# Kernel optimization log

Hardware: AMD Instinct MI355X
Metric: run time of the kernel (lower is better)

## Reference

```python
import jax, jax.numpy as jnp
import numpy as np

B, L, D = 8, 1024, 512
NB = 4              # num_blocks
DIN = 2 * D         # mamba expand=2
N = 16              # d_state
DTR = 32            # dt_rank = ceil(D/16)
DCONV = 4           # mamba depthwise conv kernel
FF = 2 * D          # ffn_expand=2
EPS = 1e-5


def setup_inputs() -> dict:
    key = jax.random.key(0)
    ks = iter(jax.random.split(key, 64))

    def rnd(shape, s=0.02):
        return jax.random.normal(next(ks), shape, jnp.float32) * s

    p = {}
    p["x"] = jax.random.normal(next(ks), (B, L, D), jnp.float32)
    # TemporalConvBlock (Conv1d D->D, k=3, pad=1, groups=1) + LayerNorm
    p["tconv_w"] = rnd((D, D, 3), 0.05)
    p["tconv_b"] = jnp.zeros((D,), jnp.float32)
    p["tnorm_w"] = jnp.ones((D,), jnp.float32)
    p["tnorm_b"] = jnp.zeros((D,), jnp.float32)
    # per-block params, stacked on leading NB axis
    p["ln1_w"] = jnp.ones((NB, D), jnp.float32)
    p["ln1_b"] = jnp.zeros((NB, D), jnp.float32)
    p["in_proj_w"] = rnd((NB, 2 * DIN, D))          # no bias (mamba default)
    p["conv_w"] = rnd((NB, DIN, 1, DCONV), 0.1)     # depthwise causal conv
    p["conv_b"] = jnp.zeros((NB, DIN), jnp.float32)
    p["x_proj_w"] = rnd((NB, DTR + 2 * N, DIN))     # no bias
    p["dt_proj_w"] = rnd((NB, DIN, DTR), 0.1)
    p["dt_proj_b"] = jnp.log(jnp.expm1(jnp.full((NB, DIN), 0.01, jnp.float32)))
    p["A_log"] = jnp.tile(jnp.log(jnp.arange(1, N + 1, dtype=jnp.float32))[None, None, :], (NB, DIN, 1))
    p["D_param"] = jnp.ones((NB, DIN), jnp.float32)
    p["out_proj_w"] = rnd((NB, D, DIN))             # no bias
    p["ln2_w"] = jnp.ones((NB, D), jnp.float32)
    p["ln2_b"] = jnp.zeros((NB, D), jnp.float32)
    p["ffn_w1"] = rnd((NB, FF, D))
    p["ffn_b1"] = jnp.zeros((NB, FF), jnp.float32)
    p["ffn_w2"] = rnd((NB, D, FF))
    p["ffn_b2"] = jnp.zeros((NB, D), jnp.float32)
    return p


def _ln(x, w, b):
    mu = jnp.mean(x, -1, keepdims=True)
    v = jnp.mean(jnp.square(x - mu), -1, keepdims=True)
    return (x - mu) * jax.lax.rsqrt(v + EPS) * w + b


def _selective_scan(u, dt, A, Bm, C, Dp):
    # u, dt: (B,L,DIN); A: (DIN,N); Bm, C: (B,L,N); Dp: (DIN,)
    def step(h, inp):
        u_t, dt_t, B_t, C_t = inp                      # (B,DIN),(B,DIN),(B,N),(B,N)
        dA = jnp.exp(dt_t[..., None] * A)              # (B,DIN,N)
        dBu = dt_t[..., None] * B_t[:, None, :] * u_t[..., None]
        h = dA * h + dBu
        y = jnp.einsum('bdn,bn->bd', h, C_t)
        return h, y

    h0 = jnp.zeros((u.shape[0], A.shape[0], A.shape[1]), u.dtype)
    xs = (u.swapaxes(0, 1), dt.swapaxes(0, 1), Bm.swapaxes(0, 1), C.swapaxes(0, 1))
    _, ys = jax.lax.scan(step, h0, xs)                 # ys: (L,B,DIN)
    return ys.swapaxes(0, 1) + u * Dp


def _mamba(x, in_w, cw, cb, xpw, dtw, dtb, A_log, Dp, ow):
    xz = jnp.einsum('bld,ed->ble', x, in_w)            # (B,L,2*DIN)
    u, z = jnp.split(xz, 2, axis=-1)
    # causal depthwise conv over time
    uc = u.swapaxes(1, 2)                              # (B,DIN,L)
    uc = jax.lax.conv_general_dilated(
        uc, cw, (1,), [(DCONV - 1, 0)],
        feature_group_count=DIN, dimension_numbers=('NCH', 'OIH', 'NCH'))
    uc = uc + cb[None, :, None]
    u = jax.nn.silu(uc.swapaxes(1, 2))                 # (B,L,DIN)
    xdb = jnp.einsum('bld,ed->ble', u, xpw)            # (B,L,DTR+2N)
    dtr, Bm, C = jnp.split(xdb, [DTR, DTR + N], axis=-1)
    dt = jax.nn.softplus(jnp.einsum('blr,dr->bld', dtr, dtw) + dtb)
    A = -jnp.exp(A_log)
    y = _selective_scan(u, dt, A, Bm, C, Dp)
    y = y * jax.nn.silu(z)
    return jnp.einsum('bld,ed->ble', y, ow)


def reference(x, tconv_w, tconv_b, tnorm_w, tnorm_b, ln1_w, ln1_b, in_proj_w,
              conv_w, conv_b, x_proj_w, dt_proj_w, dt_proj_b, A_log, D_param,
              out_proj_w, ln2_w, ln2_b, ffn_w1, ffn_b1, ffn_w2, ffn_b2):
    # TemporalConvBlock (dropout = identity in eval)
    hc = jax.lax.conv_general_dilated(
        x.swapaxes(1, 2), tconv_w, (1,), [(1, 1)],
        dimension_numbers=('NCH', 'OIH', 'NCH'))
    hc = (hc + tconv_b[None, :, None]).swapaxes(1, 2)
    h = _ln(hc + x, tnorm_w, tnorm_b)
    # stacked MambaWithFFN blocks
    for i in range(NB):
        h = h + _mamba(_ln(h, ln1_w[i], ln1_b[i]), in_proj_w[i], conv_w[i],
                       conv_b[i], x_proj_w[i], dt_proj_w[i], dt_proj_b[i],
                       A_log[i], D_param[i], out_proj_w[i])
        hn = _ln(h, ln2_w[i], ln2_b[i])
        ff = jax.nn.gelu(jnp.einsum('bld,fd->blf', hn, ffn_w1[i]) + ffn_b1[i],
                         approximate=False)
        h = h + jnp.einsum('blf,df->bld', ff, ffn_w2[i]) + ffn_b2[i]
    return h
```

## Files before the change

kernel.cpp:

```cpp
#include <hip/hip_runtime.h>
#include <hip/hip_bf16.h>
#include <math.h>

#define B_ 8
#define L_ 1024
#define D_ 512
#define NB_ 4
#define DIN_ 1024
#define NST_ 16
#define DTR_ 32
#define FF_ 1024
#define EPS_LN 1e-5f
#define M_ (B_ * L_)

#define SC_G 16
#define SC_C 32
#define SC_LEN (L_ / SC_C)

typedef __attribute__((ext_vector_type(8))) short short8;
typedef __attribute__((ext_vector_type(4))) float f32x4;

static __device__ __forceinline__ ushort f2bf(float f) {
  union { float f; unsigned u; } v; v.f = f;
  unsigned r = v.u + 0x7FFFu + ((v.u >> 16) & 1u);
  return (ushort)(r >> 16);
}
static __device__ __forceinline__ float bf2f(ushort u) {
  union { unsigned u; float f; } v; v.u = ((unsigned)u) << 16;
  return v.f;
}

static __device__ __forceinline__ void gll16(const void* g, void* l) {
  __builtin_amdgcn_global_load_lds(
      (const __attribute__((address_space(1))) void*)g,
      (__attribute__((address_space(3))) void*)l, 16, 0, 0);
}

template <int BM, int EPI, int OUTB>
__global__ __launch_bounds__(256) void mgemm2_k(
    const ushort* __restrict__ A, const ushort* __restrict__ W,
    const float* __restrict__ bias, void* __restrict__ Cp,
    float* __restrict__ C2, int M, int N, int K, int lda, int ldc)
{
  constexpr int MI = BM / 32;
  __shared__ ushort As[BM * 64];
  __shared__ ushort Bs[128 * 64];
  const int tid = threadIdx.x;
  const int lane = tid & 63;
  const int wid = tid >> 6;
  const int wm = (wid >> 1) * (BM / 2);
  const int wn = (wid & 1) * 64;
  const int bm = blockIdx.y * BM;
  const int bn = blockIdx.x * 128;
  const int fr = lane & 15;
  const int kq = lane >> 4;

  f32x4 acc[MI][4];
#pragma unroll
  for (int i = 0; i < MI; ++i)
#pragma unroll
    for (int j = 0; j < 4; ++j) acc[i][j] = (f32x4)0.f;

  for (int k0 = 0; k0 < K; k0 += 64) {
#pragma unroll
    for (int it = 0; it < BM / 32; ++it) {
      const int sb = it * 4096 + wid * 1024 + lane * 16;
      const int row = sb >> 7;
      const int js = (sb >> 4) & 7;
      const int j2 = js ^ (row & 7);
      gll16(A + (size_t)(bm + row) * lda + k0 + j2 * 8,
            (char*)As + it * 4096 + wid * 1024);
    }
#pragma unroll
    for (int it = 0; it < 4; ++it) {
      const int sb = it * 4096 + wid * 1024 + lane * 16;
      const int row = sb >> 7;
      const int js = (sb >> 4) & 7;
      const int j2 = js ^ (row & 7);
      gll16(W + (size_t)(bn + row) * K + k0 + j2 * 8,
            (char*)Bs + it * 4096 + wid * 1024);
    }
    __syncthreads();
#pragma unroll
    for (int kk = 0; kk < 2; ++kk) {
      short8 af[MI], bf[4];
#pragma unroll
      for (int mi = 0; mi < MI; ++mi) {
        const int r = wm + mi * 16 + fr;
        af[mi] = *(const short8*)&As[r * 64 + ((((kk << 2) + kq) ^ (r & 7)) << 3)];
      }
#pragma unroll
      for (int ni = 0; ni < 4; ++ni) {
        const int r = wn + ni * 16 + fr;
        bf[ni] = *(const short8*)&Bs[r * 64 + ((((kk << 2) + kq) ^ (r & 7)) << 3)];
      }
#pragma unroll
      for (int mi = 0; mi < MI; ++mi)
#pragma unroll
        for (int ni = 0; ni < 4; ++ni)
          acc[mi][ni] = __builtin_amdgcn_mfma_f32_16x16x32_bf16(
              af[mi], bf[ni], acc[mi][ni], 0, 0, 0);
    }
    __syncthreads();
  }

#pragma unroll
  for (int mi = 0; mi < MI; ++mi) {
#pragma unroll
    for (int ni = 0; ni < 4; ++ni) {
#pragma unroll
      for (int r = 0; r < 4; ++r) {
        const int gm = bm + wm + mi * 16 + (lane >> 4) * 4 + r;
        const int gn = bn + wn + ni * 16 + fr;
        float v = acc[mi][ni][r];
        if (EPI == 6) {
          if (gn < DIN_) {
            v += bias[gn];
            v = (v > 20.f) ? v : __logf(1.f + __expf(v));
            ((float*)Cp)[(size_t)gm * DIN_ + gn] = v;
          } else if (gn < DIN_ + 2 * NST_) {
            C2[(size_t)gm * (2 * NST_) + (gn - DIN_)] = v;
          }
        } else {
          if (EPI == 2 || EPI == 5) v += bias[gn];
          if (EPI == 2) v = 0.5f * v * (1.f + erff(v * 0.70710678118654752f));
          if (OUTB) {
            ((ushort*)Cp)[(size_t)gm * ldc + gn] = f2bf(v);
          } else {
            float* pc = (float*)Cp + (size_t)gm * ldc + gn;
            if (EPI == 4 || EPI == 5) v += *pc;
            *pc = v;
          }
        }
      }
    }
  }
}

template <int MODE, int EPI, int BN, int OUTB>
__global__ __launch_bounds__(256) void mgemm_k(
    const float* __restrict__ Ap, const ushort* __restrict__ W,
    const float* __restrict__ bias, void* __restrict__ Cp,
    int M, int N, int K, int lda, int ldc)
{
  constexpr int FN = BN / 32;
  __shared__ ushort As[128 * 32];
  __shared__ ushort Bs[BN * 32];
  const int tid = threadIdx.x;
  const int lane = tid & 63;
  const int wid = tid >> 6;
  const int wm = (wid >> 1) * 64;
  const int wn = (wid & 1) * (BN / 2);
  const int bm = blockIdx.y * 128;
  const int bn = blockIdx.x * BN;
  const int fr = lane & 15;
  const int kq = lane >> 4;

  f32x4 acc[4][FN];
#pragma unroll
  for (int i = 0; i < 4; ++i)
#pragma unroll
    for (int j = 0; j < FN; ++j) acc[i][j] = (f32x4)0.f;

  for (int k0 = 0; k0 < K; k0 += 32) {
#pragma unroll
    for (int it = 0; it < 2; ++it) {
      const int idx = tid + it * 256;
      const int row = idx >> 2;
      const int j = idx & 3;
      short8 s;
      float4 v0, v1;
      if (MODE == 0) {
        const float* p = Ap + (size_t)(bm + row) * lda + k0 + j * 8;
        v0 = *(const float4*)p; v1 = *(const float4*)(p + 4);
      } else {
        const int kk = k0 + j * 8;
        const int tap = kk >> 9;
        const int dcol = kk & 511;
        const int m = bm + row;
        const int l = (m & (L_ - 1)) + tap - 1;
        if (l >= 0 && l < L_) {
          const float* p = Ap + (size_t)(m - (m & (L_ - 1)) + l) * D_ + dcol;
          v0 = *(const float4*)p; v1 = *(const float4*)(p + 4);
        } else {
          v0 = make_float4(0.f, 0.f, 0.f, 0.f); v1 = v0;
        }
      }
      s[0] = (short)f2bf(v0.x); s[1] = (short)f2bf(v0.y);
      s[2] = (short)f2bf(v0.z); s[3] = (short)f2bf(v0.w);
      s[4] = (short)f2bf(v1.x); s[5] = (short)f2bf(v1.y);
      s[6] = (short)f2bf(v1.z); s[7] = (short)f2bf(v1.w);
      *(short8*)&As[row * 32 + ((j ^ ((row >> 1) & 3)) << 3)] = s;
    }
#pragma unroll
    for (int it = 0; it < BN / 64; ++it) {
      const int idx = tid + it * 256;
      const int row = idx >> 2;
      const int j = idx & 3;
      short8 s = *(const short8*)(W + (size_t)(bn + row) * K + k0 + j * 8);
      *(short8*)&Bs[row * 32 + ((j ^ ((row >> 1) & 3)) << 3)] = s;
    }
    __syncthreads();
    short8 af[4], bfr[FN];
#pragma unroll
    for (int mi = 0; mi < 4; ++mi) {
      const int r = wm + mi * 16 + fr;
      af[mi] = *(const short8*)&As[r * 32 + ((kq ^ ((r >> 1) & 3)) << 3)];
    }
#pragma unroll
    for (int ni = 0; ni < FN; ++ni) {
      const int r = wn + ni * 16 + fr;
      bfr[ni] = *(const short8*)&Bs[r * 32 + ((kq ^ ((r >> 1) & 3)) << 3)];
    }
#pragma unroll
    for (int mi = 0; mi < 4; ++mi)
#pragma unroll
      for (int ni = 0; ni < FN; ++ni)
        acc[mi][ni] = __builtin_amdgcn_mfma_f32_16x16x32_bf16(
            af[mi], bfr[ni], acc[mi][ni], 0, 0, 0);
    __syncthreads();
  }

#pragma unroll
  for (int mi = 0; mi < 4; ++mi) {
#pragma unroll
    for (int ni = 0; ni < FN; ++ni) {
#pragma unroll
      for (int r = 0; r < 4; ++r) {
        const int gm = bm + wm + mi * 16 + (lane >> 4) * 4 + r;
        const int gn = bn + wn + ni * 16 + fr;
        float v = acc[mi][ni][r];
        if (EPI == 1) v += bias[gn];
        if (OUTB) ((ushort*)Cp)[(size_t)gm * ldc + gn] = f2bf(v);
        else ((float*)Cp)[(size_t)gm * ldc + gn] = v;
      }
    }
  }
}

template <int INB, int OUTB>
__global__ __launch_bounds__(256) void ln_k(
    const void* __restrict__ inp, const float* __restrict__ res,
    const float* __restrict__ w, const float* __restrict__ b,
    void* __restrict__ outp)
{
  const int row = blockIdx.x;
  const int t = threadIdx.x;
  float v0, v1;
  if (INB) {
    const ushort* p = (const ushort*)inp + (size_t)row * D_;
    v0 = bf2f(p[t]); v1 = bf2f(p[t + 256]);
  } else {
    const float* p = (const float*)inp + (size_t)row * D_;
    v0 = p[t]; v1 = p[t + 256];
  }
  if (res) {
    const float* r = res + (size_t)row * D_;
    v0 += r[t]; v1 += r[t + 256];
  }
  float s = v0 + v1;
  float sq = v0 * v0 + v1 * v1;
#pragma unroll
  for (int m = 1; m < 64; m <<= 1) {
    s += __shfl_xor(s, m, 64);
    sq += __shfl_xor(sq, m, 64);
  }
  __shared__ float ss[4], qq[4];
  const int wid = t >> 6;
  if ((t & 63) == 0) { ss[wid] = s; qq[wid] = sq; }
  __syncthreads();
  s = ss[0] + ss[1] + ss[2] + ss[3];
  sq = qq[0] + qq[1] + qq[2] + qq[3];
  const float mu = s * (1.f / (float)D_);
  const float var = sq * (1.f / (float)D_) - mu * mu;
  const float rs = rsqrtf(var + EPS_LN);
  const float o0 = (v0 - mu) * rs * w[t] + b[t];
  const float o1 = (v1 - mu) * rs * w[t + 256] + b[t + 256];
  if (OUTB) {
    ushort* o = (ushort*)outp + (size_t)row * D_;
    o[t] = f2bf(o0); o[t + 256] = f2bf(o1);
  } else {
    float* o = (float*)outp + (size_t)row * D_;
    o[t] = o0; o[t + 256] = o1;
  }
}

__global__ __launch_bounds__(256) void dwconv_k(
    const ushort* __restrict__ xz, const float* __restrict__ cw,
    const float* __restrict__ cb, ushort* __restrict__ u)
{
  const int idx = blockIdx.x * 256 + threadIdx.x;
  const int c8 = idx & (DIN_ / 8 - 1);
  const int bl = idx >> 7;
  const int l = bl & (L_ - 1);
  const int b0 = bl - l;
  const int c0 = c8 * 8;
  float s[8], w[8][4];
#pragma unroll
  for (int j = 0; j < 8; ++j) {
    s[j] = cb[c0 + j];
    const float4 wv = *(const float4*)(cw + (c0 + j) * 4);
    w[j][0] = wv.x; w[j][1] = wv.y; w[j][2] = wv.z; w[j][3] = wv.w;
  }
#pragma unroll
  for (int k = 0; k < 4; ++k) {
    const int ll = l + k - 3;
    if (ll >= 0) {
      const short8 v = *(const short8*)(xz + (size_t)(b0 + ll) * (2 * DIN_) + c0);
#pragma unroll
      for (int j = 0; j < 8; ++j)
        s[j] = fmaf(bf2f((ushort)v[j]), w[j][k], s[j]);
    }
  }
  short8 o;
#pragma unroll
  for (int j = 0; j < 8; ++j) {
    const float t = s[j] / (1.f + __expf(-s[j]));
    o[j] = (short)f2bf(t);
  }
  *(short8*)(u + (size_t)idx * 8) = o;
}

template <bool FAST>
static __device__ __forceinline__ void dAcalc(float dtv, float A0,
                                              const float* A, float* dA)
{
  if (FAST) {
    const float e = __expf(dtv * A0);
    dA[0] = e;
#pragma unroll
    for (int n = 1; n < 16; ++n) dA[n] = dA[n - 1] * e;
  } else {
#pragma unroll
    for (int n = 0; n < 16; ++n) dA[n] = __expf(dtv * A[n]);
  }
}

template <bool FAST>
static __device__ __forceinline__ void scan_run(
    const float* __restrict__ dt, ushort* __restrict__ u,
    const float* __restrict__ BC, const ushort* __restrict__ xz,
    const float* __restrict__ A_log,
    const float* A, const float A0, const float Dpd,
    float (*Hs)[SC_G][NST_ + 1], float (*Ss)[SC_G],
    const int tid, const int g, const int c, const int d0, const int d,
    const size_t base)
{
  const int l0 = c * SC_LEN;
  float h[16];
#pragma unroll
  for (int n = 0; n < 16; ++n) h[n] = 0.f;
  float S = 0.f;

  {
    size_t row = base + l0;
    float dtv = dt[row * DIN_ + d];
    float uv = bf2f(u[row * DIN_ + d]);
    float Bv[16];
    *(float4*)&Bv[0]  = *(const float4*)(BC + row * 32);
    *(float4*)&Bv[4]  = *(const float4*)(BC + row * 32 + 4);
    *(float4*)&Bv[8]  = *(const float4*)(BC + row * 32 + 8);
    *(float4*)&Bv[12] = *(const float4*)(BC + row * 32 + 12);
    for (int i = 0; i < SC_LEN; ++i) {
      float ndt = 0.f, nu = 0.f;
      float NBv[16];
      if (i + 1 < SC_LEN) {
        const size_t nrow = row + 1;
        ndt = dt[nrow * DIN_ + d];
        nu = bf2f(u[nrow * DIN_ + d]);
        *(float4*)&NBv[0]  = *(const float4*)(BC + nrow * 32);
        *(float4*)&NBv[4]  = *(const float4*)(BC + nrow * 32 + 4);
        *(float4*)&NBv[8]  = *(const float4*)(BC + nrow * 32 + 8);
        *(float4*)&NBv[12] = *(const float4*)(BC + nrow * 32 + 12);
      }
      S += dtv;
      const float du = dtv * uv;
      float dA[16];
      dAcalc<FAST>(dtv, A0, A, dA);
#pragma unroll
      for (int n = 0; n < 16; ++n)
        h[n] = fmaf(dA[n], h[n], du * Bv[n]);
      dtv = ndt; uv = nu;
#pragma unroll
      for (int n = 0; n < 16; ++n) Bv[n] = NBv[n];
      row += 1;
    }
  }
#pragma unroll
  for (int n = 0; n < 16; ++n) Hs[c][g][n] = h[n];
  Ss[c][g] = S;
  __syncthreads();

  if (tid < SC_G * NST_) {
    const int gg = tid >> 4;
    const int n2 = tid & 15;
    const float An = -expf(A_log[(d0 + gg) * NST_ + n2]);
    float hin = 0.f;
#pragma unroll
    for (int cc = 0; cc < SC_C; ++cc) {
      const float tmp = Hs[cc][gg][n2];
      const float P = __expf(An * Ss[cc][gg]);
      Hs[cc][gg][n2] = hin;
      hin = tmp + P * hin;
    }
  }
  __syncthreads();

#pragma unroll
  for (int n = 0; n < 16; ++n) h[n] = Hs[c][g][n];
  {
    size_t row = base + l0;
    float dtv = dt[row * DIN_ + d];
    float uv = bf2f(u[row * DIN_ + d]);
    float zv = bf2f(xz[row * (2 * DIN_) + DIN_ + d]);
    float Bv[16], Cv[16];
    *(float4*)&Bv[0]  = *(const float4*)(BC + row * 32);
    *(float4*)&Bv[4]  = *(const float4*)(BC + row * 32 + 4);
    *(float4*)&Bv[8]  = *(const float4*)(BC + row * 32 + 8);
    *(float4*)&Bv[12] = *(const float4*)(BC + row * 32 + 12);
    *(float4*)&Cv[0]  = *(const float4*)(BC + row * 32 + 16);
    *(float4*)&Cv[4]  = *(const float4*)(BC + row * 32 + 20);
    *(float4*)&Cv[8]  = *(const float4*)(BC + row * 32 + 24);
    *(float4*)&Cv[12] = *(const float4*)(BC + row * 32 + 28);
    for (int i = 0; i < SC_LEN; ++i) {
      float ndt = 0.f, nu = 0.f, nz = 0.f;
      float NBv[16], NCv[16];
      if (i + 1 < SC_LEN) {
        const size_t nrow = row + 1;
        ndt = dt[nrow * DIN_ + d];
        nu = bf2f(u[nrow * DIN_ + d]);
        nz = bf2f(xz[nrow * (2 * DIN_) + DIN_ + d]);
        *(float4*)&NBv[0]  = *(const float4*)(BC + nrow * 32);
        *(float4*)&NBv[4]  = *(const float4*)(BC + nrow * 32 + 4);
        *(float4*)&NBv[8]  = *(const float4*)(BC + nrow * 32 + 8);
        *(float4*)&NBv[12] = *(const float4*)(BC + nrow * 32 + 12);
        *(float4*)&NCv[0]  = *(const float4*)(BC + nrow * 32 + 16);
        *(float4*)&NCv[4]  = *(const float4*)(BC + nrow * 32 + 20);
        *(float4*)&NCv[8]  = *(const float4*)(BC + nrow * 32 + 24);
        *(float4*)&NCv[12] = *(const float4*)(BC + nrow * 32 + 28);
      }
      const float du = dtv * uv;
      float y = uv * Dpd;
      float dA[16];
      dAcalc<FAST>(dtv, A0, A, dA);
#pragma unroll
      for (int n = 0; n < 16; ++n) {
        h[n] = fmaf(dA[n], h[n], du * Bv[n]);
        y = fmaf(h[n], Cv[n], y);
      }
      y *= zv / (1.f + __expf(-zv));
      u[row * DIN_ + d] = f2bf(y);
      dtv = ndt; uv = nu; zv = nz;
#pragma unroll
      for (int n = 0; n < 16; ++n) { Bv[n] = NBv[n]; Cv[n] = NCv[n]; }
      row += 1;
    }
  }
}

__global__ __launch_bounds__(512) void scan5_k(
    const float* __restrict__ dt, ushort* u,
    const float* __restrict__ BC, const ushort* __restrict__ xz,
    const float* __restrict__ A_log, const float* __restrict__ Dp)
{
  const int tid = threadIdx.x;
  const int g = tid & (SC_G - 1);
  const int c = tid >> 4;
  const int b = blockIdx.x >> 6;
  const int d0 = (blockIdx.x & 63) * SC_G;
  const int d = d0 + g;

  __shared__ float Hs[SC_C][SC_G][NST_ + 1];
  __shared__ float Ss[SC_C][SC_G];
  __shared__ int slow;
  if (tid == 0) slow = 0;
  __syncthreads();

  float A[16];
#pragma unroll
  for (int n = 0; n < 16; ++n) A[n] = -expf(A_log[d * NST_ + n]);
  const float A0 = A[0];
  bool myfast = true;
#pragma unroll
  for (int n = 1; n < 16; ++n)
    myfast = myfast && (fabsf(A[n] - (float)(n + 1) * A0) <= 1e-3f * fabsf(A[n]));
  if (!myfast) slow = 1;
  __syncthreads();
  const float Dpd = Dp[d];
  const size_t base = (size_t)b * L_;

  if (slow == 0)
    scan_run<true>(dt, u, BC, xz, A_log, A, A0, Dpd, Hs, Ss, tid, g, c, d0, d, base);
  else
    scan_run<false>(dt, u, BC, xz, A_log, A, A0, Dpd, Hs, Ss, tid, g, c, d0, d, base);
}

__global__ __launch_bounds__(256) void cvt_k(const float* __restrict__ in,
                                             ushort* __restrict__ out, int n8)
{
  const int i = blockIdx.x * 256 + threadIdx.x;
  if (i >= n8) return;
  const float4 a = *(const float4*)(in + (size_t)i * 8);
  const float4 b = *(const float4*)(in + (size_t)i * 8 + 4);
  short8 s;
  s[0] = (short)f2bf(a.x); s[1] = (short)f2bf(a.y);
  s[2] = (short)f2bf(a.z); s[3] = (short)f2bf(a.w);
  s[4] = (short)f2bf(b.x); s[5] = (short)f2bf(b.y);
  s[6] = (short)f2bf(b.z); s[7] = (short)f2bf(b.w);
  *(short8*)(out + (size_t)i * 8) = s;
}

__global__ __launch_bounds__(256) void twt_k(const float* __restrict__ in,
                                             ushort* __restrict__ out)
{
  const int i = blockIdx.x * 256 + threadIdx.x;
  if (i >= D_ * D_ * 3) return;
  const int o = i / (D_ * 3);
  const int rem = i - o * (D_ * 3);
  const int d = rem / 3;
  const int tap = rem - d * 3;
  out[(size_t)o * (D_ * 3) + tap * D_ + d] = f2bf(in[i]);
}

__global__ __launch_bounds__(256) void xpT_k(const float* __restrict__ xpw,
                                             ushort* __restrict__ out)
{
  const int i = blockIdx.x * 256 + threadIdx.x;
  if (i >= DIN_ * DTR_) return;
  const int k = i >> 5;
  const int r = i & 31;
  out[i] = f2bf(xpw[(size_t)r * DIN_ + k]);
}

__global__ __launch_bounds__(256) void pack_k(const float* __restrict__ wc,
                                              const float* __restrict__ xpw,
                                              ushort* __restrict__ wbig)
{
  const int i = blockIdx.x * 256 + threadIdx.x;
  if (i >= 1152 * 1024) return;
  const int r = i >> 10;
  const int k = i & 1023;
  float v;
  if (r < 1024) v = wc[i];
  else if (r < 1056) v = xpw[(size_t)(DTR_ + r - 1024) * DIN_ + k];
  else v = 0.f;
  wbig[i] = f2bf(v);
}

extern "C" void kernel_launch(void* const* d_in, const int* in_sizes, int n_in,
                              void* d_out, int out_size, void* d_ws, size_t ws_size,
                              hipStream_t stream)
{
  const float* x         = (const float*)d_in[0];
  const float* tconv_w   = (const float*)d_in[1];
  const float* tconv_b   = (const float*)d_in[2];
  const float* tnorm_w   = (const float*)d_in[3];
  const float* tnorm_b   = (const float*)d_in[4];
  const float* ln1_w     = (const float*)d_in[5];
  const float* ln1_b     = (const float*)d_in[6];
  const float* in_proj_w = (const float*)d_in[7];
  const float* conv_w    = (const float*)d_in[8];
  const float* conv_b    = (const float*)d_in[9];
  const float* x_proj_w  = (const float*)d_in[10];
  const float* dt_proj_w = (const float*)d_in[11];
  const float* dt_proj_b = (const float*)d_in[12];
  const float* A_log     = (const float*)d_in[13];
  const float* D_param   = (const float*)d_in[14];
  const float* out_proj_w= (const float*)d_in[15];
  const float* ln2_w     = (const float*)d_in[16];
  const float* ln2_b     = (const float*)d_in[17];
  const float* ffn_w1    = (const float*)d_in[18];
  const float* ffn_b1    = (const float*)d_in[19];
  const float* ffn_w2    = (const float*)d_in[20];
  const float* ffn_b2    = (const float*)d_in[21];

  float* h = (float*)d_out;

  char* p = (char*)d_ws;
  ushort* wTT  = (ushort*)p; p += (size_t)512 * 1536 * 2;
  ushort* wIP  = (ushort*)p; p += (size_t)4 * 2048 * 512 * 2;
  ushort* wOP  = (ushort*)p; p += (size_t)4 * 512 * 1024 * 2;
  ushort* wF1  = (ushort*)p; p += (size_t)4 * 1024 * 512 * 2;
  ushort* wF2  = (ushort*)p; p += (size_t)4 * 512 * 1024 * 2;
  ushort* xpwT = (ushort*)p; p += (size_t)4 * 1024 * 32 * 2;
  ushort* wBig = (ushort*)p; p += (size_t)4 * 1152 * 1024 * 2;
  float*  wcT  = (float*)p;  p += (size_t)1024 * 1024 * 4;
  ushort* xin  = (ushort*)p; p += (size_t)M_ * 512 * 2;
  ushort* xzb  = (ushort*)p; p += (size_t)M_ * 2048 * 2;
  ushort* ubuf = (ushort*)p; p += (size_t)M_ * 1024 * 2;
  float*  bc   = (float*)p;  p += (size_t)M_ * 32 * 4;
  float*  dtb  = (float*)p;  p += (size_t)M_ * 1024 * 4;
  ushort* ff   = (ushort*)p; p += (size_t)M_ * 1024 * 2;

  const dim3 blk(256);

  cvt_k<<<dim3(4 * 2048 * 512 / 8 / 256), blk, 0, stream>>>(in_proj_w, wIP, 4 * 2048 * 512 / 8);
  cvt_k<<<dim3(4 * 512 * 1024 / 8 / 256), blk, 0, stream>>>(out_proj_w, wOP, 4 * 512 * 1024 / 8);
  cvt_k<<<dim3(4 * 1024 * 512 / 8 / 256), blk, 0, stream>>>(ffn_w1, wF1, 4 * 1024 * 512 / 8);
  cvt_k<<<dim3(4 * 512 * 1024 / 8 / 256), blk, 0, stream>>>(ffn_w2, wF2, 4 * 512 * 1024 / 8);
  twt_k<<<dim3((D_ * D_ * 3 + 255) / 256), blk, 0, stream>>>(tconv_w, wTT);
  for (int i = 0; i < NB_; ++i)
    xpT_k<<<dim3(DIN_ * DTR_ / 256), blk, 0, stream>>>(
        x_proj_w + (size_t)i * 64 * DIN_, xpwT + (size_t)i * DIN_ * DTR_);
  for (int i = 0; i < NB_; ++i) {
    mgemm_k<0, 0, 128, 0><<<dim3(8, 8), blk, 0, stream>>>(
        dt_proj_w + (size_t)i * DIN_ * DTR_, xpwT + (size_t)i * DIN_ * DTR_,
        nullptr, wcT, 1024, 1024, 32, 32, 1024);
    pack_k<<<dim3(1152 * 1024 / 256), blk, 0, stream>>>(
        wcT, x_proj_w + (size_t)i * 64 * DIN_, wBig + (size_t)i * 1152 * 1024);
  }

  mgemm_k<1, 1, 64, 1><<<dim3(8, 64), blk, 0, stream>>>(
      x, wTT, tconv_b, xin, M_, 512, 1536, 0, 512);
  ln_k<1, 0><<<dim3(M_), blk, 0, stream>>>(xin, x, tnorm_w, tnorm_b, h);

  for (int i = 0; i < NB_; ++i) {
    ln_k<0, 1><<<dim3(M_), blk, 0, stream>>>(h, nullptr, ln1_w + i * D_, ln1_b + i * D_, xin);
    mgemm2_k<128, 0, 1><<<dim3(16, 64), blk, 0, stream>>>(
        xin, wIP + (size_t)i * 2048 * 512, nullptr, xzb, nullptr,
        M_, 2048, 512, 512, 2048);
    dwconv_k<<<dim3(M_ * DIN_ / 8 / 256), blk, 0, stream>>>(
        xzb, conv_w + (size_t)i * DIN_ * 4, conv_b + (size_t)i * DIN_, ubuf);
    mgemm2_k<128, 6, 0><<<dim3(9, 64), blk, 0, stream>>>(
        ubuf, wBig + (size_t)i * 1152 * 1024, dt_proj_b + (size_t)i * DIN_,
        dtb, bc, M_, 1152, 1024, 1024, 1024);
    scan5_k<<<dim3(B_ * (DIN_ / SC_G)), dim3(512), 0, stream>>>(
        dtb, ubuf, bc, xzb, A_log + (size_t)i * DIN_ * NST_, D_param + (size_t)i * DIN_);
    mgemm2_k<64, 4, 0><<<dim3(4, 128), blk, 0, stream>>>(
        ubuf, wOP + (size_t)i * 512 * 1024, nullptr, h, nullptr,
        M_, 512, 1024, 1024, 512);
    ln_k<0, 1><<<dim3(M_), blk, 0, stream>>>(h, nullptr, ln2_w + i * D_, ln2_b + i * D_, xin);
    mgemm2_k<128, 2, 1><<<dim3(8, 64), blk, 0, stream>>>(
        xin, wF1 + (size_t)i * 1024 * 512, ffn_b1 + (size_t)i * FF_, ff, nullptr,
        M_, 1024, 512, 512, 1024);
    mgemm2_k<64, 5, 0><<<dim3(4, 128), blk, 0, stream>>>(
        ff, wF2 + (size_t)i * 512 * 1024, ffn_b2 + (size_t)i * D_, h, nullptr,
        M_, 512, 1024, 1024, 512);
  }
}
```

Before: 1.390 ms.

## Store dt/BC in bf16, pad conv input, swizzle GEMM grid, simplify scan

Several changes at once. The dt and B/C scan inputs are now stored as bf16 instead of fp32, cutting scan memory traffic, and the temporal conv moves onto the async-LDS mgemm2 path using a zero-padded bf16 copy of x. GEMM workgroup IDs are remapped across groups of 8 for better cache locality, and some GEMM BM tiles drop to 64 for more blocks. The scan drops its manual software prefetch in favour of unrolled loops and computes the dA powers with a shallower dependency chain. These add bf16 rounding error on dt, B and C, and the grid remap assumes the block count divides by 8.

```diff
diff --git a/kernel.cpp b/kernel.cpp
--- a/kernel.cpp
+++ b/kernel.cpp
@@ -36,11 +36,11 @@
       (__attribute__((address_space(3))) void*)l, 16, 0, 0);
 }
 
-template <int BM, int EPI, int OUTB>
+template <int MODE, int BM, int EPI, int OUTB>
 __global__ __launch_bounds__(256) void mgemm2_k(
     const ushort* __restrict__ A, const ushort* __restrict__ W,
     const float* __restrict__ bias, void* __restrict__ Cp,
-    float* __restrict__ C2, int M, int N, int K, int lda, int ldc)
+    ushort* __restrict__ C2, int M, int N, int K, int lda, int ldc)
 {
   constexpr int MI = BM / 32;
   __shared__ ushort As[BM * 64];
@@ -50,8 +50,14 @@
   const int wid = tid >> 6;
   const int wm = (wid >> 1) * (BM / 2);
   const int wn = (wid & 1) * 64;
-  const int bm = blockIdx.y * BM;
-  const int bn = blockIdx.x * 128;
+
+  const int gx = gridDim.x;
+  const int nwg = gx * gridDim.y;
+  int wg = blockIdx.y * gx + blockIdx.x;
+  wg = (wg & 7) * (nwg >> 3) + (wg >> 3);
+  const int bm = (wg / gx) * BM;
+  const int bn = (wg % gx) * 128;
+
   const int fr = lane & 15;
   const int kq = lane >> 4;
 
@@ -68,8 +74,19 @@
       const int row = sb >> 7;
       const int js = (sb >> 4) & 7;
       const int j2 = js ^ (row & 7);
-      gll16(A + (size_t)(bm + row) * lda + k0 + j2 * 8,
-            (char*)As + it * 4096 + wid * 1024);
+      const ushort* src;
+      if (MODE == 0) {
+        src = A + (size_t)(bm + row) * lda + k0 + j2 * 8;
+      } else {
+        const int k = k0 + j2 * 8;
+        const int tap = k >> 9;
+        const int dcol = k & 511;
+        const int m = bm + row;
+        const int bq = m >> 10;
+        const int l = m & (L_ - 1);
+        src = A + ((size_t)bq * (L_ + 2) + l + tap) * D_ + dcol;
+      }
+      gll16(src, (char*)As + it * 4096 + wid * 1024);
     }
 #pragma unroll
     for (int it = 0; it < 4; ++it) {
@@ -117,12 +134,12 @@
           if (gn < DIN_) {
             v += bias[gn];
             v = (v > 20.f) ? v : __logf(1.f + __expf(v));
-            ((float*)Cp)[(size_t)gm * DIN_ + gn] = v;
+            ((ushort*)Cp)[(size_t)gm * DIN_ + gn] = f2bf(v);
           } else if (gn < DIN_ + 2 * NST_) {
-            C2[(size_t)gm * (2 * NST_) + (gn - DIN_)] = v;
+            C2[(size_t)gm * (2 * NST_) + (gn - DIN_)] = f2bf(v);
           }
         } else {
-          if (EPI == 2 || EPI == 5) v += bias[gn];
+          if (EPI == 1 || EPI == 2 || EPI == 5) v += bias[gn];
           if (EPI == 2) v = 0.5f * v * (1.f + erff(v * 0.70710678118654752f));
           if (OUTB) {
             ((ushort*)Cp)[(size_t)gm * ldc + gn] = f2bf(v);
@@ -137,7 +154,7 @@
   }
 }
 
-template <int MODE, int EPI, int BN, int OUTB>
+template <int EPI, int BN, int OUTB>
 __global__ __launch_bounds__(256) void mgemm_k(
     const float* __restrict__ Ap, const ushort* __restrict__ W,
     const float* __restrict__ bias, void* __restrict__ Cp,
@@ -169,23 +186,9 @@
       const int row = idx >> 2;
       const int j = idx & 3;
       short8 s;
-      float4 v0, v1;
-      if (MODE == 0) {
-        const float* p = Ap + (size_t)(bm + row) * lda + k0 + j * 8;
-        v0 = *(const float4*)p; v1 = *(const float4*)(p + 4);
-      } else {
-        const int kk = k0 + j * 8;
-        const int tap = kk >> 9;
-        const int dcol = kk & 511;
-        const int m = bm + row;
-        const int l = (m & (L_ - 1)) + tap - 1;
-        if (l >= 0 && l < L_) {
-          const float* p = Ap + (size_t)(m - (m & (L_ - 1)) + l) * D_ + dcol;
-          v0 = *(const float4*)p; v1 = *(const float4*)(p + 4);
-        } else {
-          v0 = make_float4(0.f, 0.f, 0.f, 0.f); v1 = v0;
-        }
-      }
+      const float* p = Ap + (size_t)(bm + row) * lda + k0 + j * 8;
+      const float4 v0 = *(const float4*)p;
+      const float4 v1 = *(const float4*)(p + 4);
       s[0] = (short)f2bf(v0.x); s[1] = (short)f2bf(v0.y);
       s[2] = (short)f2bf(v0.z); s[3] = (short)f2bf(v0.w);
       s[4] = (short)f2bf(v1.x); s[5] = (short)f2bf(v1.y);
@@ -326,20 +329,39 @@
                                               const float* A, float* dA)
 {
   if (FAST) {
-    const float e = __expf(dtv * A0);
-    dA[0] = e;
-#pragma unroll
-    for (int n = 1; n < 16; ++n) dA[n] = dA[n - 1] * e;
+    const float e1 = __expf(dtv * A0);
+    const float e2 = e1 * e1, e4 = e2 * e2, e8 = e4 * e4, e16 = e8 * e8;
+#pragma unroll
+    for (int n = 0; n < 16; ++n) {
+      const int pp = n + 1;
+      float v = 1.f;
+      if (pp & 1) v *= e1;
+      if (pp & 2) v *= e2;
+      if (pp & 4) v *= e4;
+      if (pp & 8) v *= e8;
+      if (pp & 16) v *= e16;
+      dA[n] = v;
+    }
   } else {
 #pragma unroll
     for (int n = 0; n < 16; ++n) dA[n] = __expf(dtv * A[n]);
+  }
+}
+
+static __device__ __forceinline__ void ldbf16x16(const ushort* p, float* dst) {
+  const short8 s0 = *(const short8*)p;
+  const short8 s1 = *(const short8*)(p + 8);
+#pragma unroll
+  for (int n = 0; n < 8; ++n) {
+    dst[n] = bf2f((ushort)s0[n]);
+    dst[n + 8] = bf2f((ushort)s1[n]);
   }
 }
 
 template <bool FAST>
 static __device__ __forceinline__ void scan_run(
-    const float* __restrict__ dt, ushort* __restrict__ u,
-    const float* __restrict__ BC, const ushort* __restrict__ xz,
+    const ushort* __restrict__ dt, ushort* __restrict__ u,
+    const ushort* __restrict__ BC, const ushort* __restrict__ xz,
     const float* __restrict__ A_log,
     const float* A, const float A0, const float Dpd,
     float (*Hs)[SC_G][NST_ + 1], float (*Ss)[SC_G],
@@ -352,39 +374,20 @@
   for (int n = 0; n < 16; ++n) h[n] = 0.f;
   float S = 0.f;
 
-  {
-    size_t row = base + l0;
-    float dtv = dt[row * DIN_ + d];
-    float uv = bf2f(u[row * DIN_ + d]);
+#pragma unroll 4
+  for (int i = 0; i < SC_LEN; ++i) {
+    const size_t row = base + l0 + i;
+    const float dtv = bf2f(dt[row * DIN_ + d]);
+    const float uv = bf2f(u[row * DIN_ + d]);
     float Bv[16];
-    *(float4*)&Bv[0]  = *(const float4*)(BC + row * 32);
-    *(float4*)&Bv[4]  = *(const float4*)(BC + row * 32 + 4);
-    *(float4*)&Bv[8]  = *(const float4*)(BC + row * 32 + 8);
-    *(float4*)&Bv[12] = *(const float4*)(BC + row * 32 + 12);
-    for (int i = 0; i < SC_LEN; ++i) {
-      float ndt = 0.f, nu = 0.f;
-      float NBv[16];
-      if (i + 1 < SC_LEN) {
-        const size_t nrow = row + 1;
-        ndt = dt[nrow * DIN_ + d];
-        nu = bf2f(u[nrow * DIN_ + d]);
-        *(float4*)&NBv[0]  = *(const float4*)(BC + nrow * 32);
-        *(float4*)&NBv[4]  = *(const float4*)(BC + nrow * 32 + 4);
-        *(float4*)&NBv[8]  = *(const float4*)(BC + nrow * 32 + 8);
-        *(float4*)&NBv[12] = *(const float4*)(BC + nrow * 32 + 12);
-      }
-      S += dtv;
-      const float du = dtv * uv;
-      float dA[16];
-      dAcalc<FAST>(dtv, A0, A, dA);
-#pragma unroll
-      for (int n = 0; n < 16; ++n)
-        h[n] = fmaf(dA[n], h[n], du * Bv[n]);
-      dtv = ndt; uv = nu;
-#pragma unroll
-      for (int n = 0; n < 16; ++n) Bv[n] = NBv[n];
-      row += 1;
-    }
+    ldbf16x16(BC + row * 32, Bv);
+    S += dtv;
+    const float du = dtv * uv;
+    float dA[16];
+    dAcalc<FAST>(dtv, A0, A, dA);
+#pragma unroll
+    for (int n = 0; n < 16; ++n)
+      h[n] = fmaf(dA[n], h[n], du * Bv[n]);
   }
 #pragma unroll
   for (int n = 0; n < 16; ++n) Hs[c][g][n] = h[n];
@@ -408,59 +411,32 @@
 
 #pragma unroll
   for (int n = 0; n < 16; ++n) h[n] = Hs[c][g][n];
-  {
-    size_t row = base + l0;
-    float dtv = dt[row * DIN_ + d];
-    float uv = bf2f(u[row * DIN_ + d]);
-    float zv = bf2f(xz[row * (2 * DIN_) + DIN_ + d]);
+#pragma unroll 4
+  for (int i = 0; i < SC_LEN; ++i) {
+    const size_t row = base + l0 + i;
+    const float dtv = bf2f(dt[row * DIN_ + d]);
+    const float uv = bf2f(u[row * DIN_ + d]);
+    const float zv = bf2f(xz[row * (2 * DIN_) + DIN_ + d]);
     float Bv[16], Cv[16];
-    *(float4*)&Bv[0]  = *(const float4*)(BC + row * 32);
-    *(float4*)&Bv[4]  = *(const float4*)(BC + row * 32 + 4);
-    *(float4*)&Bv[8]  = *(const float4*)(BC + row * 32 + 8);
-    *(float4*)&Bv[12] = *(const float4*)(BC + row * 32 + 12);
-    *(float4*)&Cv[0]  = *(const float4*)(BC + row * 32 + 16);
-    *(float4*)&Cv[4]  = *(const float4*)(BC + row * 32 + 20);
-    *(float4*)&Cv[8]  = *(const float4*)(BC + row * 32 + 24);
-    *(float4*)&Cv[12] = *(const float4*)(BC + row * 32 + 28);
-    for (int i = 0; i < SC_LEN; ++i) {
-      float ndt = 0.f, nu = 0.f, nz = 0.f;
-      float NBv[16], NCv[16];
-      if (i + 1 < SC_LEN) {
-        const size_t nrow = row + 1;
-        ndt = dt[nrow * DIN_ + d];
-        nu = bf2f(u[nrow * DIN_ + d]);
-        nz = bf2f(xz[nrow * (2 * DIN_) + DIN_ + d]);
-        *(float4*)&NBv[0]  = *(const float4*)(BC + nrow * 32);
-        *(float4*)&NBv[4]  = *(const float4*)(BC + nrow * 32 + 4);
-        *(float4*)&NBv[8]  = *(const float4*)(BC + nrow * 32 + 8);
-        *(float4*)&NBv[12] = *(const float4*)(BC + nrow * 32 + 12);
-        *(float4*)&NCv[0]  = *(const float4*)(BC + nrow * 32 + 16);
-        *(float4*)&NCv[4]  = *(const float4*)(BC + nrow * 32 + 20);
-        *(float4*)&NCv[8]  = *(const float4*)(BC + nrow * 32 + 24);
-        *(float4*)&NCv[12] = *(const float4*)(BC + nrow * 32 + 28);
-      }
-      const float du = dtv * uv;
-      float y = uv * Dpd;
-      float dA[16];
-      dAcalc<FAST>(dtv, A0, A, dA);
-#pragma unroll
-      for (int n = 0; n < 16; ++n) {
-        h[n] = fmaf(dA[n], h[n], du * Bv[n]);
-        y = fmaf(h[n], Cv[n], y);
-      }
-      y *= zv / (1.f + __expf(-zv));
-      u[row * DIN_ + d] = f2bf(y);
-      dtv = ndt; uv = nu; zv = nz;
-#pragma unroll
-      for (int n = 0; n < 16; ++n) { Bv[n] = NBv[n]; Cv[n] = NCv[n]; }
-      row += 1;
-    }
-  }
-}
-
-__global__ __launch_bounds__(512) void scan5_k(
-    const float* __restrict__ dt, ushort* u,
-    const float* __restrict__ BC, const ushort* __restrict__ xz,
+    ldbf16x16(BC + row * 32, Bv);
+    ldbf16x16(BC + row * 32 + 16, Cv);
+    const float du = dtv * uv;
+    float y = uv * Dpd;
+    float dA[16];
+    dAcalc<FAST>(dtv, A0, A, dA);
+#pragma unroll
+    for (int n = 0; n < 16; ++n) {
+      h[n] = fmaf(dA[n], h[n], du * Bv[n]);
+      y = fmaf(h[n], Cv[n], y);
+    }
+    y *= zv / (1.f + __expf(-zv));
+    u[row * DIN_ + d] = f2bf(y);
+  }
+}
+
+__global__ __launch_bounds__(512) void scan6_k(
+    const ushort* __restrict__ dt, ushort* u,
+    const ushort* __restrict__ BC, const ushort* __restrict__ xz,
     const float* __restrict__ A_log, const float* __restrict__ Dp)
 {
   const int tid = threadIdx.x;
@@ -508,6 +484,27 @@
   s[4] = (short)f2bf(b.x); s[5] = (short)f2bf(b.y);
   s[6] = (short)f2bf(b.z); s[7] = (short)f2bf(b.w);
   *(short8*)(out + (size_t)i * 8) = s;
+}
+
+__global__ __launch_bounds__(256) void padx_k(const float* __restrict__ x,
+                                              ushort* __restrict__ xpad)
+{
+  const int i = blockIdx.x * 256 + threadIdx.x;
+  const int row = i >> 6;
+  const int c0 = (i & 63) * 8;
+  const int b = row / (L_ + 2);
+  const int r = row - b * (L_ + 2);
+  short8 s = {0, 0, 0, 0, 0, 0, 0, 0};
+  if (r != 0 && r != L_ + 1) {
+    const float* p = x + ((size_t)b * L_ + (r - 1)) * D_ + c0;
+    const float4 a = *(const float4*)p;
+    const float4 bb = *(const float4*)(p + 4);
+    s[0] = (short)f2bf(a.x); s[1] = (short)f2bf(a.y);
+    s[2] = (short)f2bf(a.z); s[3] = (short)f2bf(a.w);
+    s[4] = (short)f2bf(bb.x); s[5] = (short)f2bf(bb.y);
+    s[6] = (short)f2bf(bb.z); s[7] = (short)f2bf(bb.w);
+  }
+  *(short8*)(xpad + (size_t)row * D_ + c0) = s;
 }
 
 __global__ __launch_bounds__(256) void twt_k(const float* __restrict__ in,
@@ -585,11 +582,12 @@
   ushort* xpwT = (ushort*)p; p += (size_t)4 * 1024 * 32 * 2;
   ushort* wBig = (ushort*)p; p += (size_t)4 * 1152 * 1024 * 2;
   float*  wcT  = (float*)p;  p += (size_t)1024 * 1024 * 4;
+  ushort* xpad = (ushort*)p; p += (size_t)B_ * (L_ + 2) * D_ * 2;
   ushort* xin  = (ushort*)p; p += (size_t)M_ * 512 * 2;
   ushort* xzb  = (ushort*)p; p += (size_t)M_ * 2048 * 2;
   ushort* ubuf = (ushort*)p; p += (size_t)M_ * 1024 * 2;
-  float*  bc   = (float*)p;  p += (size_t)M_ * 32 * 4;
-  float*  dtb  = (float*)p;  p += (size_t)M_ * 1024 * 4;
+  ushort* bc   = (ushort*)p; p += (size_t)M_ * 32 * 2;
+  ushort* dtb  = (ushort*)p; p += (size_t)M_ * 1024 * 2;
   ushort* ff   = (ushort*)p; p += (size_t)M_ * 1024 * 2;
 
   const dim3 blk(256);
@@ -599,41 +597,42 @@
   cvt_k<<<dim3(4 * 1024 * 512 / 8 / 256), blk, 0, stream>>>(ffn_w1, wF1, 4 * 1024 * 512 / 8);
   cvt_k<<<dim3(4 * 512 * 1024 / 8 / 256), blk, 0, stream>>>(ffn_w2, wF2, 4 * 512 * 1024 / 8);
   twt_k<<<dim3((D_ * D_ * 3 + 255) / 256), blk, 0, stream>>>(tconv_w, wTT);
+  padx_k<<<dim3(B_ * (L_ + 2) * D_ / 8 / 256), blk, 0, stream>>>(x, xpad);
   for (int i = 0; i < NB_; ++i)
     xpT_k<<<dim3(DIN_ * DTR_ / 256), blk, 0, stream>>>(
         x_proj_w + (size_t)i * 64 * DIN_, xpwT + (size_t)i * DIN_ * DTR_);
   for (int i = 0; i < NB_; ++i) {
-    mgemm_k<0, 0, 128, 0><<<dim3(8, 8), blk, 0, stream>>>(
+    mgemm_k<0, 128, 0><<<dim3(8, 8), blk, 0, stream>>>(
         dt_proj_w + (size_t)i * DIN_ * DTR_, xpwT + (size_t)i * DIN_ * DTR_,
         nullptr, wcT, 1024, 1024, 32, 32, 1024);
     pack_k<<<dim3(1152 * 1024 / 256), blk, 0, stream>>>(
         wcT, x_proj_w + (size_t)i * 64 * DIN_, wBig + (size_t)i * 1152 * 1024);
   }
 
-  mgemm_k<1, 1, 64, 1><<<dim3(8, 64), blk, 0, stream>>>(
-      x, wTT, tconv_b, xin, M_, 512, 1536, 0, 512);
+  mgemm2_k<1, 128, 1, 1><<<dim3(4, 64), blk, 0, stream>>>(
+      xpad, wTT, tconv_b, xin, nullptr, M_, 512, 1536, 0, 512);
   ln_k<1, 0><<<dim3(M_), blk, 0, stream>>>(xin, x, tnorm_w, tnorm_b, h);
 
   for (int i = 0; i < NB_; ++i) {
     ln_k<0, 1><<<dim3(M_), blk, 0, stream>>>(h, nullptr, ln1_w + i * D_, ln1_b + i * D_, xin);
-    mgemm2_k<128, 0, 1><<<dim3(16, 64), blk, 0, stream>>>(
+    mgemm2_k<0, 128, 0, 1><<<dim3(16, 64), blk, 0, stream>>>(
         xin, wIP + (size_t)i * 2048 * 512, nullptr, xzb, nullptr,
         M_, 2048, 512, 512, 2048);
     dwconv_k<<<dim3(M_ * DIN_ / 8 / 256), blk, 0, stream>>>(
         xzb, conv_w + (size_t)i * DIN_ * 4, conv_b + (size_t)i * DIN_, ubuf);
-    mgemm2_k<128, 6, 0><<<dim3(9, 64), blk, 0, stream>>>(
+    mgemm2_k<0, 64, 6, 0><<<dim3(9, 128), blk, 0, stream>>>(
         ubuf, wBig + (size_t)i * 1152 * 1024, dt_proj_b + (size_t)i * DIN_,
         dtb, bc, M_, 1152, 1024, 1024, 1024);
-    scan5_k<<<dim3(B_ * (DIN_ / SC_G)), dim3(512), 0, stream>>>(
+    scan6_k<<<dim3(B_ * (DIN_ / SC_G)), dim3(512), 0, stream>>>(
         dtb, ubuf, bc, xzb, A_log + (size_t)i * DIN_ * NST_, D_param + (size_t)i * DIN_);
-    mgemm2_k<64, 4, 0><<<dim3(4, 128), blk, 0, stream>>>(
+    mgemm2_k<0, 64, 4, 0><<<dim3(4, 128), blk, 0, stream>>>(
         ubuf, wOP + (size_t)i * 512 * 1024, nullptr, h, nullptr,
         M_, 512, 1024, 1024, 512);
     ln_k<0, 1><<<dim3(M_), blk, 0, stream>>>(h, nullptr, ln2_w + i * D_, ln2_b + i * D_, xin);
-    mgemm2_k<128, 2, 1><<<dim3(8, 64), blk, 0, stream>>>(
+    mgemm2_k<0, 64, 2, 1><<<dim3(8, 128), blk, 0, stream>>>(
         xin, wF1 + (size_t)i * 1024 * 512, ffn_b1 + (size_t)i * FF_, ff, nullptr,
         M_, 1024, 512, 512, 1024);
-    mgemm2_k<64, 5, 0><<<dim3(4, 128), blk, 0, stream>>>(
+    mgemm2_k<0, 64, 5, 0><<<dim3(4, 128), blk, 0, stream>>>(
         ff, wF2 + (size_t)i * 512 * 1024, ffn_b2 + (size_t)i * D_, h, nullptr,
         M_, 512, 1024, 1024, 512);
   }
```

Result: faster. 1.236 ms (-11.1%).
